# Optimization experiments

Measured on AMD Instinct MI355X. Metric: run time of the kernel, lower is better.

## Reference

```python
import jax, jax.numpy as jnp
import numpy as np

N_HEAD = 16

def setup_inputs() -> dict:
    key = jax.random.key(0)
    ks = jax.random.split(key, 9)
    B, T, C = 1, 4096, 1024
    s = 1.0 / np.sqrt(C)
    x = jax.random.normal(ks[0], (B, T, C), dtype=jnp.float32)
    Wq = jax.random.uniform(ks[1], (C, C), jnp.float32, -s, s)
    bq = jax.random.uniform(ks[2], (C,), jnp.float32, -s, s)
    Wk = jax.random.uniform(ks[3], (C, C), jnp.float32, -s, s)
    bk = jax.random.uniform(ks[4], (C,), jnp.float32, -s, s)
    Wv = jax.random.uniform(ks[5], (C, C), jnp.float32, -s, s)
    bv = jax.random.uniform(ks[6], (C,), jnp.float32, -s, s)
    Wp = jax.random.uniform(ks[7], (C, C), jnp.float32, -s, s)
    bp = jax.random.uniform(ks[8], (C,), jnp.float32, -s, s)
    return {"x": x, "Wq": Wq, "bq": bq, "Wk": Wk, "bk": bk,
            "Wv": Wv, "bv": bv, "Wp": Wp, "bp": bp}

def reference(x, Wq, bq, Wk, bk, Wv, bv, Wp, bp):
    B, T, C = x.shape
    H = N_HEAD
    D = C // H
    # projections -> (B, H, T, D)
    def proj(W, b):
        return (x @ W.T + b).reshape(B, T, H, D).transpose(0, 2, 1, 3)
    q, k, v = proj(Wq, bq), proj(Wk, bk), proj(Wv, bv)
    scale = 1.0 / np.sqrt(D).astype(np.float32)
    att = jnp.einsum('bhtd,bhsd->bhts', q, k) * scale  # (B,H,T,T)
    causal = jnp.tril(jnp.ones((T, T), dtype=bool))
    att = jnp.where(causal[None, None], att, -jnp.inf)
    att = jax.nn.softmax(att, axis=-1)
    y = jnp.einsum('bhts,bhsd->bhtd', att, v)  # (B,H,T,D)
    y = y.transpose(0, 2, 1, 3).reshape(B, T, C)
    return y @ Wp.T + bp
```

## Files before the change

kernel.cpp:

```cpp
#include <hip/hip_runtime.h>
#include <hip/hip_bf16.h>
#include <math.h>

typedef __bf16 bf16x8 __attribute__((ext_vector_type(8)));
typedef __bf16 bf16x4 __attribute__((ext_vector_type(4)));
typedef float f32x4 __attribute__((ext_vector_type(4)));

#define MFMA_BF16 __builtin_amdgcn_mfma_f32_16x16x32_bf16

#define QSCALE 0.18033688011112042f

__device__ inline void async_load16(const __hip_bfloat16* g, __hip_bfloat16* l) {
    __builtin_amdgcn_global_load_lds(
        (const __attribute__((address_space(1))) unsigned int*)g,
        (__attribute__((address_space(3))) unsigned int*)l,
        16, 0, 0);
}

__device__ inline int sig(int x) {
    return (x & ~12) | ((x & 4) << 1) | ((x & 8) >> 1);
}

__device__ inline unsigned int pack_bf16_trunc(float lo, float hi) {
    return __builtin_amdgcn_perm(__float_as_uint(hi), __float_as_uint(lo),
                                 0x07060302u);
}

__global__ __launch_bounds__(256) void convert_all(
    const float* __restrict__ x,
    const float* __restrict__ Wq, const float* __restrict__ Wk,
    const float* __restrict__ Wv, const float* __restrict__ Wp,
    __hip_bfloat16* __restrict__ xb,
    __hip_bfloat16* __restrict__ Wqb, __hip_bfloat16* __restrict__ Wkb,
    __hip_bfloat16* __restrict__ Wvb, __hip_bfloat16* __restrict__ Wpb,
    int nx, int nw)
{
    const int xblocks = nx >> 11;
    const int wblocks = nw >> 11;
    int b = blockIdx.x;
    const float* in;
    __hip_bfloat16* out;
    int i;
    if (b < xblocks) {
        in = x; out = xb; i = (b * 256 + threadIdx.x) * 8;
    } else {
        b -= xblocks;
        const int w = b / wblocks, bb = b - w * wblocks;
        in  = w == 0 ? Wq : w == 1 ? Wk : w == 2 ? Wv : Wp;
        out = w == 0 ? Wqb : w == 1 ? Wkb : w == 2 ? Wvb : Wpb;
        i = (bb * 256 + threadIdx.x) * 8;
    }
    const float4 a = *(const float4*)(in + i);
    const float4 c = *(const float4*)(in + i + 4);
    __hip_bfloat16 tmp[8];
    tmp[0] = __float2bfloat16(a.x); tmp[1] = __float2bfloat16(a.y);
    tmp[2] = __float2bfloat16(a.z); tmp[3] = __float2bfloat16(a.w);
    tmp[4] = __float2bfloat16(c.x); tmp[5] = __float2bfloat16(c.y);
    tmp[6] = __float2bfloat16(c.z); tmp[7] = __float2bfloat16(c.w);
    *(bf16x8*)(out + i) = *(const bf16x8*)tmp;
}

__global__ __launch_bounds__(256) void gemm_qkv(
    const __hip_bfloat16* __restrict__ A,
    const __hip_bfloat16* __restrict__ B,
    const float* __restrict__ bq, const float* __restrict__ bk, const float* __restrict__ bv,
    __hip_bfloat16* __restrict__ Qo, __hip_bfloat16* __restrict__ Ko,
    __hip_bfloat16* __restrict__ Vt,
    int M, int K)
{
    __shared__ __align__(16) __hip_bfloat16 smem[2 * 128 * 64];
    __hip_bfloat16* As = smem;
    __hip_bfloat16* Bs = smem + 128 * 64;

    const int tid  = threadIdx.x;
    const int lane = tid & 63;
    const int wave = tid >> 6;
    const int l15  = lane & 15;
    const int quad = lane >> 4;
    const int m0 = blockIdx.x * 128;
    const int n0 = blockIdx.y * 128;
    const int wr = wave >> 1, wc = wave & 1;
    const int sel = n0 >> 10;

    f32x4 acc[4][4] = {};

    int srow[4], scol[4];
    #pragma unroll
    for (int i = 0; i < 4; ++i) {
        const int c = tid + 256 * i;
        srow[i] = c >> 3;
        scol[i] = ((c & 7) ^ (srow[i] & 7)) * 8;
    }

    for (int k0 = 0; k0 < K; k0 += 64) {
        __syncthreads();
        #pragma unroll
        for (int i = 0; i < 4; ++i) {
            async_load16(A + (size_t)(m0 + srow[i]) * K + k0 + scol[i],
                         As + (size_t)(tid + 256 * i) * 8);
            async_load16(B + (size_t)(n0 + srow[i]) * K + k0 + scol[i],
                         Bs + (size_t)(tid + 256 * i) * 8);
        }
        __syncthreads();

        #pragma unroll
        for (int kd = 0; kd < 2; ++kd) {
            bf16x8 af[4], bfr[4];
            #pragma unroll
            for (int mi = 0; mi < 4; ++mi) {
                const int row = wr * 64 + mi * 16 + l15;
                af[mi] = *(const bf16x8*)(
                    As + row * 64 + (((kd * 4 + quad) ^ (row & 7)) << 3));
            }
            #pragma unroll
            for (int ni = 0; ni < 4; ++ni) {
                const int row = wc * 64 + ni * 16 + l15;
                bfr[ni] = *(const bf16x8*)(
                    Bs + row * 64 + (((kd * 4 + quad) ^ (row & 7)) << 3));
            }
            #pragma unroll
            for (int mi = 0; mi < 4; ++mi)
                #pragma unroll
                for (int ni = 0; ni < 4; ++ni)
                    acc[mi][ni] = MFMA_BF16(af[mi], bfr[ni], acc[mi][ni], 0, 0, 0);
        }
    }

    if (sel == 2) {
        __syncthreads();
        #pragma unroll
        for (int ni = 0; ni < 4; ++ni) {
            const int lc = wc * 64 + ni * 16 + l15;
            const float bias = bv[(n0 + lc) & 1023];
            #pragma unroll
            for (int mi = 0; mi < 4; ++mi) {
                const int mb = wr * 64 + mi * 16 + quad * 4;
                const int g = mb >> 3, off = mb & 7;
                __hip_bfloat16 t[4];
                #pragma unroll
                for (int r = 0; r < 4; ++r)
                    t[r] = __float2bfloat16(acc[mi][ni][r] + bias);
                *(bf16x4*)(smem + lc * 128 + ((g ^ (lc & 15)) << 3) + off)
                    = *(const bf16x4*)t;
            }
        }
        __syncthreads();
        const int cc0 = n0 & 1023;
        #pragma unroll
        for (int i = 0; i < 8; ++i) {
            const int q = tid + 256 * i;
            const int ch = q >> 4, mg = q & 15;
            bf16x8 v = *(const bf16x8*)(smem + ch * 128 + ((mg ^ (ch & 15)) << 3));
            *(bf16x8*)(Vt + (size_t)(cc0 + ch) * M + m0 + mg * 8) = v;
        }
    } else {
        __hip_bfloat16* dst = sel == 0 ? Qo : Ko;
        const float* bptr   = sel == 0 ? bq : bk;
        const float sc      = sel == 0 ? QSCALE : 1.0f;
        #pragma unroll
        for (int ni = 0; ni < 4; ++ni) {
            const int cc = (n0 + wc * 64 + ni * 16 + l15) & 1023;
            const float bias = bptr[cc];
            #pragma unroll
            for (int mi = 0; mi < 4; ++mi) {
                const int row = m0 + wr * 64 + mi * 16 + quad * 4;
                #pragma unroll
                for (int r = 0; r < 4; ++r)
                    dst[(size_t)(row + r) * 1024 + cc] =
                        __float2bfloat16((acc[mi][ni][r] + bias) * sc);
            }
        }
    }
}

__global__ __launch_bounds__(256) void gemm_out_f32(
    const __hip_bfloat16* __restrict__ A,
    const __hip_bfloat16* __restrict__ B,
    const float* __restrict__ bias,
    float* __restrict__ Cf,
    int M, int N, int K)
{
    __shared__ __align__(16) __hip_bfloat16 As[64 * 64];
    __shared__ __align__(16) __hip_bfloat16 Bs[128 * 64];

    const int tid  = threadIdx.x;
    const int lane = tid & 63;
    const int wave = tid >> 6;
    const int l15  = lane & 15;
    const int quad = lane >> 4;
    const int m0 = blockIdx.x * 64;
    const int n0 = blockIdx.y * 128;
    const int wr = wave >> 1, wc = wave & 1;

    f32x4 acc[2][4] = {};

    int srow[4], scol[4];
    #pragma unroll
    for (int i = 0; i < 4; ++i) {
        const int c = tid + 256 * i;
        srow[i] = c >> 3;
        scol[i] = ((c & 7) ^ (srow[i] & 7)) * 8;
    }

    for (int k0 = 0; k0 < K; k0 += 64) {
        __syncthreads();
        #pragma unroll
        for (int i = 0; i < 2; ++i)
            async_load16(A + (size_t)(m0 + srow[i]) * K + k0 + scol[i],
                         As + (size_t)(tid + 256 * i) * 8);
        #pragma unroll
        for (int i = 0; i < 4; ++i)
            async_load16(B + (size_t)(n0 + srow[i]) * K + k0 + scol[i],
                         Bs + (size_t)(tid + 256 * i) * 8);
        __syncthreads();

        #pragma unroll
        for (int kd = 0; kd < 2; ++kd) {
            bf16x8 af[2], bfr[4];
            #pragma unroll
            for (int mi = 0; mi < 2; ++mi) {
                const int row = wr * 32 + mi * 16 + l15;
                af[mi] = *(const bf16x8*)(
                    As + row * 64 + (((kd * 4 + quad) ^ (row & 7)) << 3));
            }
            #pragma unroll
            for (int ni = 0; ni < 4; ++ni) {
                const int row = wc * 64 + ni * 16 + l15;
                bfr[ni] = *(const bf16x8*)(
                    Bs + row * 64 + (((kd * 4 + quad) ^ (row & 7)) << 3));
            }
            #pragma unroll
            for (int mi = 0; mi < 2; ++mi)
                #pragma unroll
                for (int ni = 0; ni < 4; ++ni)
                    acc[mi][ni] = MFMA_BF16(af[mi], bfr[ni], acc[mi][ni], 0, 0, 0);
        }
    }

    #pragma unroll
    for (int ni = 0; ni < 4; ++ni) {
        const int col = n0 + wc * 64 + ni * 16 + l15;
        const float bv = bias[col];
        #pragma unroll
        for (int mi = 0; mi < 2; ++mi) {
            const int row = m0 + wr * 32 + mi * 16 + quad * 4;
            #pragma unroll
            for (int r = 0; r < 4; ++r)
                Cf[(size_t)(row + r) * N + col] = acc[mi][ni][r] + bv;
        }
    }
}

__global__ __launch_bounds__(512, 4) void attn_causal(
    const __hip_bfloat16* __restrict__ Q,
    const __hip_bfloat16* __restrict__ K,
    const __hip_bfloat16* __restrict__ Vt,
    __hip_bfloat16* __restrict__ PoB,
    float* __restrict__ PlB,
    int T, int C)
{
    const int nwg  = (int)(gridDim.x * gridDim.y);
    const int chunk = nwg >> 3;
    const int lin  = (int)(blockIdx.x + gridDim.x * blockIdx.y);
    const int work = (lin & 7) * chunk + (lin >> 3);
    const int h  = work >> 5;
    const int bx = work & 31;
    const int j  = bx & 7;
    const int sq = bx >> 3;
    const int tid  = threadIdx.x;
    const int w    = tid >> 6;
    const int lane = tid & 63;
    const int l15  = lane & 15;
    const int quad = lane >> 4;

    const size_t TCs = (size_t)T * C;
    const size_t HT  = (size_t)T * 16;
    __hip_bfloat16* Po = PoB + (size_t)sq * TCs;
    float* Pl = PlB + (size_t)sq * HT;

    const int len1 = j + 1, len2 = 16 - j;
    const int tile1 = j,    tile2 = 15 - j;
    const int kb1 = len1 * sq, kb2 = len2 * sq;

    __shared__ __align__(16) __hip_bfloat16 Ks[4][64 * 64];
    __shared__ __align__(16) __hip_bfloat16 Vts[4][64 * 64];

    const int r0 = tid >> 3, g0 = ((tid & 7) ^ (r0 & 7)) * 8;
    const __hip_bfloat16* Kg0 = K + (size_t)sig(r0) * C + h * 64 + g0;
    const __hip_bfloat16* Vg0 = Vt + (size_t)(h * 64 + r0) * T + g0;

    int koff[2][4], voff[2][4];
    #pragma unroll
    for (int kd = 0; kd < 2; ++kd)
        #pragma unroll
        for (int sb = 0; sb < 4; ++sb) {
            const int kappa = 32 * (sb & 1) + 8 * (l15 >> 2) + 4 * (sb >> 1) + (l15 & 3);
            const int rho = sig(kappa);
            koff[kd][sb] = rho * 64 + (((kd * 4 + quad) ^ (rho & 7)) << 3);
        }
    #pragma unroll
    for (int kk = 0; kk < 2; ++kk)
        #pragma unroll
        for (int db = 0; db < 4; ++db) {
            const int vrow = db * 16 + l15;
            voff[kk][db] = vrow * 64 + (((kk * 4 + quad) ^ (vrow & 7)) << 3);
        }

    bf16x8 ones;
    #pragma unroll
    for (int jj = 0; jj < 8; ++jj) ones[jj] = (__bf16)1.0f;

    int qbase = tile1 * 256 + w * 32;
    bf16x8 aq[2][2];
    #pragma unroll
    for (int rb = 0; rb < 2; ++rb)
        #pragma unroll
        for (int kd = 0; kd < 2; ++kd)
            aq[rb][kd] = *(const bf16x8*)(
                Q + (size_t)(qbase + rb * 16 + l15) * C + h * 64 + kd * 32 + quad * 8);

    f32x4 o[2][4] = {};
    f32x4 lacc[2] = {};

    auto stage = [&](int idx) {
        const int kb = (idx < len1) ? (kb1 + idx) : (kb2 + idx - len1);
        const size_t so = (size_t)kb << 6;
        const int sl = idx & 3;
        async_load16(Kg0 + so * C, &Ks[sl][tid * 8]);
        async_load16(Vg0 + so, &Vts[sl][tid * 8]);
    };

    stage(0);
    stage(1);

    for (int it = 0; it < 17; ++it) {
        if (it + 2 < 17) stage(it + 2);
        if (it < 15)
            asm volatile("s_waitcnt vmcnt(4)\n\ts_barrier" ::: "memory");
        else if (it == 15)
            asm volatile("s_waitcnt vmcnt(2)\n\ts_barrier" ::: "memory");
        else
            asm volatile("s_waitcnt vmcnt(0)\n\ts_barrier" ::: "memory");

        const int cur = it & 3;
        const int kb = (it < len1) ? (kb1 + it) : (kb2 + it - len1);
        const int s0 = kb << 6;

        if (it == len1) {
            #pragma unroll
            for (int rb = 0; rb < 2; ++rb) {
                const int row = qbase + rb * 16 + l15;
                #pragma unroll
                for (int db = 0; db < 4; ++db) {
                    __hip_bfloat16 t[4];
                    #pragma unroll
                    for (int r = 0; r < 4; ++r)
                        t[r] = __float2bfloat16(o[rb][db][r]);
                    *(bf16x4*)(Po + (size_t)row * C + h * 64 + db * 16 + quad * 4)
                        = *(const bf16x4*)t;
                    o[rb][db] = (f32x4){0.f, 0.f, 0.f, 0.f};
                }
                if (quad == 0)
                    Pl[(size_t)h * T + row] = lacc[rb][0];
                lacc[rb] = (f32x4){0.f, 0.f, 0.f, 0.f};
            }
            qbase = tile2 * 256 + w * 32;
            #pragma unroll
            for (int rb = 0; rb < 2; ++rb)
                #pragma unroll
                for (int kd = 0; kd < 2; ++kd)
                    aq[rb][kd] = *(const bf16x8*)(
                        Q + (size_t)(qbase + rb * 16 + l15) * C + h * 64 + kd * 32 + quad * 8);
        }

        if (s0 <= qbase + 31) {
            f32x4 sv[2][4] = {};
            #pragma unroll
            for (int kd = 0; kd < 2; ++kd)
                #pragma unroll
                for (int sb = 0; sb < 4; ++sb) {
                    bf16x8 ak = *(const bf16x8*)(&Ks[cur][koff[kd][sb]]);
                    sv[0][sb] = MFMA_BF16(ak, aq[0][kd], sv[0][sb], 0, 0, 0);
                    sv[1][sb] = MFMA_BF16(ak, aq[1][kd], sv[1][sb], 0, 0, 0);
                }

            const bool diag = (s0 + 63 > qbase);
            bf16x8 bp[2][2];
            #pragma unroll
            for (int rb = 0; rb < 2; ++rb) {
                float pv[4][4];
                #pragma unroll
                for (int sb = 0; sb < 4; ++sb)
                    #pragma unroll
                    for (int r = 0; r < 4; ++r)
                        pv[sb][r] = __builtin_amdgcn_exp2f(sv[rb][sb][r]);
                if (diag) {
                    const int thr = qbase + rb * 16 + l15 - s0 - 8 * quad;
                    #pragma unroll
                    for (int sb = 0; sb < 4; ++sb)
                        #pragma unroll
                        for (int r = 0; r < 4; ++r) {
                            const int c = 32 * (sb & 1) + 4 * (sb >> 1) + r;
                            pv[sb][r] = (c <= thr) ? pv[sb][r] : 0.f;
                        }
                }
                #pragma unroll
                for (int kk = 0; kk < 2; ++kk) {
                    union { unsigned int u[4]; bf16x8 v; } pk;
                    pk.u[0] = pack_bf16_trunc(pv[kk][0], pv[kk][1]);
                    pk.u[1] = pack_bf16_trunc(pv[kk][2], pv[kk][3]);
                    pk.u[2] = pack_bf16_trunc(pv[kk + 2][0], pv[kk + 2][1]);
                    pk.u[3] = pack_bf16_trunc(pv[kk + 2][2], pv[kk + 2][3]);
                    bp[rb][kk] = pk.v;
                }
            }

            lacc[0] = MFMA_BF16(ones, bp[0][0], lacc[0], 0, 0, 0);
            lacc[0] = MFMA_BF16(ones, bp[0][1], lacc[0], 0, 0, 0);
            lacc[1] = MFMA_BF16(ones, bp[1][0], lacc[1], 0, 0, 0);
            lacc[1] = MFMA_BF16(ones, bp[1][1], lacc[1], 0, 0, 0);

            #pragma unroll
            for (int kk = 0; kk < 2; ++kk)
                #pragma unroll
                for (int db = 0; db < 4; ++db) {
                    bf16x8 av = *(const bf16x8*)(&Vts[cur][voff[kk][db]]);
                    o[0][db] = MFMA_BF16(av, bp[0][kk], o[0][db], 0, 0, 0);
                    o[1][db] = MFMA_BF16(av, bp[1][kk], o[1][db], 0, 0, 0);
                }
        }
    }

    #pragma unroll
    for (int rb = 0; rb < 2; ++rb) {
        const int row = qbase + rb * 16 + l15;
        #pragma unroll
        for (int db = 0; db < 4; ++db) {
            __hip_bfloat16 t[4];
            #pragma unroll
            for (int r = 0; r < 4; ++r)
                t[r] = __float2bfloat16(o[rb][db][r]);
            *(bf16x4*)(Po + (size_t)row * C + h * 64 + db * 16 + quad * 4)
                = *(const bf16x4*)t;
        }
        if (quad == 0)
            Pl[(size_t)h * T + row] = lacc[rb][0];
    }
}

__global__ __launch_bounds__(256) void merge_y(
    const __hip_bfloat16* __restrict__ PoB, const float* __restrict__ PlB,
    __hip_bfloat16* __restrict__ Y, int T, int C)
{
    const size_t i = ((size_t)blockIdx.x * 256 + threadIdx.x) * 8;
    const int row = (int)(i / C);
    const int h   = ((int)(i % C)) >> 6;
    const size_t TC = (size_t)T * C;
    const size_t HT = (size_t)T * 16;
    float acc[8] = {};
    float l = 0.f;
    #pragma unroll
    for (int z = 0; z < 4; ++z) {
        bf16x8 a = *(const bf16x8*)(PoB + z * TC + i);
        #pragma unroll
        for (int r = 0; r < 8; ++r)
            acc[r] += (float)(((const __bf16*)&a)[r]);
        l += PlB[z * HT + (size_t)h * T + row];
    }
    const float inv = 1.0f / l;
    __hip_bfloat16 t[8];
    #pragma unroll
    for (int r = 0; r < 8; ++r)
        t[r] = __float2bfloat16(acc[r] * inv);
    *(bf16x8*)(Y + i) = *(const bf16x8*)t;
}

extern "C" void kernel_launch(void* const* d_in, const int* in_sizes, int n_in,
                              void* d_out, int out_size, void* d_ws, size_t ws_size,
                              hipStream_t stream)
{
    const float* x  = (const float*)d_in[0];
    const float* Wq = (const float*)d_in[1];
    const float* bq = (const float*)d_in[2];
    const float* Wk = (const float*)d_in[3];
    const float* bk = (const float*)d_in[4];
    const float* Wv = (const float*)d_in[5];
    const float* bv = (const float*)d_in[6];
    const float* Wp = (const float*)d_in[7];
    const float* bp = (const float*)d_in[8];

    const int C = 1024;
    const int T = in_sizes[0] / C;
    const int H = 16;
    const size_t TC = (size_t)T * C;
    const size_t CC = (size_t)C * C;

    __hip_bfloat16* xb  = (__hip_bfloat16*)d_ws;
    __hip_bfloat16* Wqb = xb + TC;
    __hip_bfloat16* Wkb = Wqb + CC;
    __hip_bfloat16* Wvb = Wkb + CC;
    __hip_bfloat16* Wpb = Wvb + CC;
    __hip_bfloat16* Qw  = Wpb + CC;
    __hip_bfloat16* Kw  = Qw + TC;
    __hip_bfloat16* Vtw = Kw + TC;
    __hip_bfloat16* PoB = Vtw + TC;
    float* PlB = (float*)(PoB + 4 * TC);
    __hip_bfloat16* Yw  = xb;
    float* out = (float*)d_out;

    convert_all<<<(int)(TC / 2048 + 4 * CC / 2048), 256, 0, stream>>>(
        x, Wq, Wk, Wv, Wp, xb, Wqb, Wkb, Wvb, Wpb, (int)TC, (int)CC);

    gemm_qkv<<<dim3(T / 128, 3072 / 128), 256, 0, stream>>>(
        xb, Wqb, bq, bk, bv, Qw, Kw, Vtw, T, C);

    attn_causal<<<dim3(32, H), 512, 0, stream>>>(
        Qw, Kw, Vtw, PoB, PlB, T, C);

    merge_y<<<(int)(TC / 8 / 256), 256, 0, stream>>>(
        PoB, PlB, Yw, T, C);

    gemm_out_f32<<<dim3(T / 64, C / 128), 256, 0, stream>>>(
        Yw, Wpb, bp, out, T, C, C);
}
```

Before: 199.4 us.

## Double-buffer LDS tiles in both GEMMs and use 512 threads for QKV

Both projection GEMMs now keep two LDS stages and issue the async global-to-LDS loads for the next K tile before computing on the current one. Each iteration uses a single waitcnt plus barrier in place of two __syncthreads, so load latency can overlap MFMA work. The QKV GEMM also moves from 4 to 8 waves per block, with each wave owning a 32x64 sub-tile. That halves accumulator registers per thread but doubles LDS use per block, which may reduce how many blocks fit on a CU.

After: 185.2 us, median of 3. 7.1% less time.

```diff
diff --git a/kernel.cpp b/kernel.cpp
--- a/kernel.cpp
+++ b/kernel.cpp
@@ -60,7 +60,7 @@
     *(bf16x8*)(out + i) = *(const bf16x8*)tmp;
 }
 
-__global__ __launch_bounds__(256) void gemm_qkv(
+__global__ __launch_bounds__(512) void gemm_qkv(
     const __hip_bfloat16* __restrict__ A,
     const __hip_bfloat16* __restrict__ B,
     const float* __restrict__ bq, const float* __restrict__ bk, const float* __restrict__ bv,
@@ -68,9 +68,7 @@
     __hip_bfloat16* __restrict__ Vt,
     int M, int K)
 {
-    __shared__ __align__(16) __hip_bfloat16 smem[2 * 128 * 64];
-    __hip_bfloat16* As = smem;
-    __hip_bfloat16* Bs = smem + 128 * 64;
+    __shared__ __align__(16) __hip_bfloat16 smem[2][2 * 128 * 64];
 
     const int tid  = threadIdx.x;
     const int lane = tid & 63;
@@ -79,36 +77,48 @@
     const int quad = lane >> 4;
     const int m0 = blockIdx.x * 128;
     const int n0 = blockIdx.y * 128;
-    const int wr = wave >> 1, wc = wave & 1;
+    const int wr = wave >> 1;
+    const int wc = wave & 1;
     const int sel = n0 >> 10;
 
-    f32x4 acc[4][4] = {};
-
-    int srow[4], scol[4];
-    #pragma unroll
-    for (int i = 0; i < 4; ++i) {
-        const int c = tid + 256 * i;
+    f32x4 acc[2][4] = {};
+
+    int srow[2], scol[2];
+    #pragma unroll
+    for (int i = 0; i < 2; ++i) {
+        const int c = tid + 512 * i;
         srow[i] = c >> 3;
         scol[i] = ((c & 7) ^ (srow[i] & 7)) * 8;
     }
 
-    for (int k0 = 0; k0 < K; k0 += 64) {
-        __syncthreads();
-        #pragma unroll
-        for (int i = 0; i < 4; ++i) {
+    auto stageg = [&](int k0, int buf) {
+        __hip_bfloat16* As = smem[buf];
+        __hip_bfloat16* Bs = smem[buf] + 128 * 64;
+        #pragma unroll
+        for (int i = 0; i < 2; ++i) {
             async_load16(A + (size_t)(m0 + srow[i]) * K + k0 + scol[i],
-                         As + (size_t)(tid + 256 * i) * 8);
+                         As + (size_t)(tid + 512 * i) * 8);
             async_load16(B + (size_t)(n0 + srow[i]) * K + k0 + scol[i],
-                         Bs + (size_t)(tid + 256 * i) * 8);
-        }
-        __syncthreads();
+                         Bs + (size_t)(tid + 512 * i) * 8);
+        }
+    };
+
+    const int NK = K >> 6;
+    stageg(0, 0);
+
+    for (int kt = 0; kt < NK; ++kt) {
+        asm volatile("s_waitcnt vmcnt(0)\n\ts_barrier" ::: "memory");
+        if (kt + 1 < NK) stageg((kt + 1) * 64, (kt + 1) & 1);
+
+        const __hip_bfloat16* As = smem[kt & 1];
+        const __hip_bfloat16* Bs = smem[kt & 1] + 128 * 64;
 
         #pragma unroll
         for (int kd = 0; kd < 2; ++kd) {
-            bf16x8 af[4], bfr[4];
-            #pragma unroll
-            for (int mi = 0; mi < 4; ++mi) {
-                const int row = wr * 64 + mi * 16 + l15;
+            bf16x8 af[2], bfr[4];
+            #pragma unroll
+            for (int mi = 0; mi < 2; ++mi) {
+                const int row = wr * 32 + mi * 16 + l15;
                 af[mi] = *(const bf16x8*)(
                     As + row * 64 + (((kd * 4 + quad) ^ (row & 7)) << 3));
             }
@@ -119,7 +129,7 @@
                     Bs + row * 64 + (((kd * 4 + quad) ^ (row & 7)) << 3));
             }
             #pragma unroll
-            for (int mi = 0; mi < 4; ++mi)
+            for (int mi = 0; mi < 2; ++mi)
                 #pragma unroll
                 for (int ni = 0; ni < 4; ++ni)
                     acc[mi][ni] = MFMA_BF16(af[mi], bfr[ni], acc[mi][ni], 0, 0, 0);
@@ -127,30 +137,31 @@
     }
 
     if (sel == 2) {
+        __hip_bfloat16* tsm = smem[0];
         __syncthreads();
         #pragma unroll
         for (int ni = 0; ni < 4; ++ni) {
             const int lc = wc * 64 + ni * 16 + l15;
             const float bias = bv[(n0 + lc) & 1023];
             #pragma unroll
-            for (int mi = 0; mi < 4; ++mi) {
-                const int mb = wr * 64 + mi * 16 + quad * 4;
+            for (int mi = 0; mi < 2; ++mi) {
+                const int mb = wr * 32 + mi * 16 + quad * 4;
                 const int g = mb >> 3, off = mb & 7;
                 __hip_bfloat16 t[4];
                 #pragma unroll
                 for (int r = 0; r < 4; ++r)
                     t[r] = __float2bfloat16(acc[mi][ni][r] + bias);
-                *(bf16x4*)(smem + lc * 128 + ((g ^ (lc & 15)) << 3) + off)
+                *(bf16x4*)(tsm + lc * 128 + ((g ^ (lc & 15)) << 3) + off)
                     = *(const bf16x4*)t;
             }
         }
         __syncthreads();
         const int cc0 = n0 & 1023;
         #pragma unroll
-        for (int i = 0; i < 8; ++i) {
-            const int q = tid + 256 * i;
+        for (int i = 0; i < 4; ++i) {
+            const int q = tid + 512 * i;
             const int ch = q >> 4, mg = q & 15;
-            bf16x8 v = *(const bf16x8*)(smem + ch * 128 + ((mg ^ (ch & 15)) << 3));
+            bf16x8 v = *(const bf16x8*)(tsm + ch * 128 + ((mg ^ (ch & 15)) << 3));
             *(bf16x8*)(Vt + (size_t)(cc0 + ch) * M + m0 + mg * 8) = v;
         }
     } else {
@@ -162,8 +173,8 @@
             const int cc = (n0 + wc * 64 + ni * 16 + l15) & 1023;
             const float bias = bptr[cc];
             #pragma unroll
-            for (int mi = 0; mi < 4; ++mi) {
-                const int row = m0 + wr * 64 + mi * 16 + quad * 4;
+            for (int mi = 0; mi < 2; ++mi) {
+                const int row = m0 + wr * 32 + mi * 16 + quad * 4;
                 #pragma unroll
                 for (int r = 0; r < 4; ++r)
                     dst[(size_t)(row + r) * 1024 + cc] =
@@ -180,8 +191,7 @@
     float* __restrict__ Cf,
     int M, int N, int K)
 {
-    __shared__ __align__(16) __hip_bfloat16 As[64 * 64];
-    __shared__ __align__(16) __hip_bfloat16 Bs[128 * 64];
+    __shared__ __align__(16) __hip_bfloat16 smem[2][(64 + 128) * 64];
 
     const int tid  = threadIdx.x;
     const int lane = tid & 63;
@@ -202,8 +212,9 @@
         scol[i] = ((c & 7) ^ (srow[i] & 7)) * 8;
     }
 
-    for (int k0 = 0; k0 < K; k0 += 64) {
-        __syncthreads();
+    auto stageg = [&](int k0, int buf) {
+        __hip_bfloat16* As = smem[buf];
+        __hip_bfloat16* Bs = smem[buf] + 64 * 64;
         #pragma unroll
         for (int i = 0; i < 2; ++i)
             async_load16(A + (size_t)(m0 + srow[i]) * K + k0 + scol[i],
@@ -212,7 +223,17 @@
         for (int i = 0; i < 4; ++i)
             async_load16(B + (size_t)(n0 + srow[i]) * K + k0 + scol[i],
                          Bs + (size_t)(tid + 256 * i) * 8);
-        __syncthreads();
+    };
+
+    const int NK = K >> 6;
+    stageg(0, 0);
+
+    for (int kt = 0; kt < NK; ++kt) {
+        asm volatile("s_waitcnt vmcnt(0)\n\ts_barrier" ::: "memory");
+        if (kt + 1 < NK) stageg((kt + 1) * 64, (kt + 1) & 1);
+
+        const __hip_bfloat16* As = smem[kt & 1];
+        const __hip_bfloat16* Bs = smem[kt & 1] + 64 * 64;
 
         #pragma unroll
         for (int kd = 0; kd < 2; ++kd) {
@@ -511,7 +532,7 @@
     convert_all<<<(int)(TC / 2048 + 4 * CC / 2048), 256, 0, stream>>>(
         x, Wq, Wk, Wv, Wp, xb, Wqb, Wkb, Wvb, Wpb, (int)TC, (int)CC);
 
-    gemm_qkv<<<dim3(T / 128, 3072 / 128), 256, 0, stream>>>(
+    gemm_qkv<<<dim3(T / 128, 3072 / 128), 512, 0, stream>>>(
         xb, Wqb, bq, bk, bv, Qw, Kw, Vtw, T, C);
 
     attn_causal<<<dim3(32, H), 512, 0, stream>>>(
```
